# Kernel optimization log

Measured on AMD Instinct MI355X. Metric: run time of the kernel, lower is better.

## Reference

```python
import jax, jax.numpy as jnp
import numpy as np
import math

NUM_HEADS = 8
KEY_SIZE = 512
EMBED_DIM = 256
BN_EPS = 1e-5


def batchnorm2d_train(x, w, b):
    # x: [B, H, N, hd]; channel axis = 1 (heads). Training-mode batch stats
    # over (B, N, hd), biased variance, as in torch BatchNorm2d forward.
    mean = jnp.mean(x, axis=(0, 2, 3), keepdims=True)
    var = jnp.mean((x - mean) ** 2, axis=(0, 2, 3), keepdims=True)
    xn = (x - mean) * jax.lax.rsqrt(var + BN_EPS)
    return xn * w[None, :, None, None] + b[None, :, None, None]


def l2_normalize(x, axis, eps=1e-12):
    # matches F.normalize(p=2): x / max(||x||, eps)
    n = jnp.sqrt(jnp.sum(x * x, axis=axis, keepdims=True))
    return x / jnp.maximum(n, eps)


def sparsemax(z, axis):
    # Euclidean projection onto the simplex along `axis` (Martins & Astudillo).
    K = z.shape[axis]
    z = z - jnp.max(z, axis=axis, keepdims=True)  # shift-invariant, for stability
    zs = jnp.flip(jnp.sort(z, axis=axis), axis=axis)  # descending sort
    rng_shape = [1] * z.ndim
    rng_shape[axis] = K
    rng = jnp.arange(1, K + 1, dtype=z.dtype).reshape(rng_shape)
    css = jnp.cumsum(zs, axis=axis)
    support = (1.0 + rng * zs) > css
    k_z = jnp.sum(support.astype(jnp.int32), axis=axis, keepdims=True)  # support size >= 1
    tau_sum = jnp.take_along_axis(css, k_z - 1, axis=axis)
    tau = (tau_sum - 1.0) / k_z.astype(z.dtype)
    return jnp.maximum(z - tau, 0.0)


def setup_inputs() -> dict:
    key = jax.random.key(0)
    k1, k2, k3 = jax.random.split(key, 3)
    B, N, C = 8, 1024, EMBED_DIM
    lim = 1.0 / math.sqrt(C)  # torch Linear default init range
    x = jax.random.normal(k1, (B, N, C), dtype=jnp.float32)
    qw = jax.random.uniform(k2, (KEY_SIZE, C), jnp.float32, -lim, lim)
    kw = jax.random.uniform(k3, (KEY_SIZE, C), jnp.float32, -lim, lim)
    bn_weight = jnp.ones((NUM_HEADS,), jnp.float32)
    bn_bias = jnp.zeros((NUM_HEADS,), jnp.float32)
    return {"x": x, "qw": qw, "kw": kw, "bn_weight": bn_weight, "bn_bias": bn_bias}


def reference(x, qw, kw, bn_weight, bn_bias):
    B, N, C = x.shape
    H = NUM_HEADS
    hd = KEY_SIZE // H
    q = jnp.einsum('bnc,kc->bnk', x, qw)  # [B,N,key_size]
    k = jnp.einsum('bnc,kc->bnk', x, kw)
    Q = q.reshape(B, N, H, hd).transpose(0, 2, 1, 3)  # [B,H,N,hd]
    K = k.reshape(B, N, H, hd).transpose(0, 2, 1, 3)
    Q = batchnorm2d_train(Q, bn_weight, bn_bias)
    K = batchnorm2d_train(K, bn_weight, bn_bias)
    Q = l2_normalize(Q, axis=3)
    K = l2_normalize(K, axis=3)
    scores = jnp.einsum('bhnd,bhmd->bhnm', Q, K) / math.sqrt(C)  # scale by sqrt(embeded_dim)
    scores = scores.transpose(0, 2, 1, 3).reshape(B, N, H * N)  # [B,N,H*N]
    # dropout is identity in eval mode
    return sparsemax(scores, axis=1)
```

## Files before the change

### kernel.cpp

```cpp
#include <hip/hip_runtime.h>
#include <math.h>

#define S_STAT 0
#define S_Q    32
#define S_K    (32 + 4194304)
#define S_PL   (32 + 8388608)
#define PLSZ   4194304

typedef unsigned short ushort;
typedef unsigned int uint;
typedef __attribute__((ext_vector_type(8))) short short8;
typedef __attribute__((ext_vector_type(16))) float floatx16;

__device__ __forceinline__ float wave_sum(float v) {
#pragma unroll
    for (int m = 1; m < 64; m <<= 1) v += __shfl_xor(v, m);
    return v;
}

__device__ __forceinline__ ushort f2bf(float f) {
    uint u = __float_as_uint(f);
    uint r = (u + 0x7fffu + ((u >> 16) & 1u)) >> 16;
    return (ushort)r;
}

__global__ __launch_bounds__(64) void k0_zero(float* __restrict__ ws) {
    if (threadIdx.x < 32) ws[S_STAT + threadIdx.x] = 0.0f;
}

__global__ __launch_bounds__(256) void k1_gemm(const float* __restrict__ x,
                                               const float* __restrict__ qw,
                                               const float* __restrict__ kw,
                                               float* __restrict__ ws) {
    __shared__ float xa[64][20];
    __shared__ float wb[64][20];
    __shared__ float red[8];
    const int t  = threadIdx.x;
    const int n0 = blockIdx.x * 64;
    const int ty = blockIdx.y;
    const bool is_q = (ty < 8);
    const int j0 = (ty & 7) * 64;
    const float* __restrict__ W = is_q ? qw : kw;
    float* __restrict__ outp = ws + (is_q ? S_Q : S_K);

    const int lr = t >> 2;
    const int lc = (t & 3) * 4;
    const int tr = (t >> 4) * 4;
    const int tc = (t & 15) * 4;

    float acc[4][4];
#pragma unroll
    for (int i = 0; i < 4; ++i)
#pragma unroll
        for (int j = 0; j < 4; ++j) acc[i][j] = 0.0f;

    for (int kc = 0; kc < 256; kc += 16) {
        __syncthreads();
        *(float4*)(&xa[lr][lc]) = *(const float4*)(x + (size_t)(n0 + lr) * 256 + kc + lc);
        *(float4*)(&wb[lr][lc]) = *(const float4*)(W + (size_t)(j0 + lr) * 256 + kc + lc);
        __syncthreads();
#pragma unroll
        for (int k4 = 0; k4 < 16; k4 += 4) {
            float4 av[4], bv[4];
#pragma unroll
            for (int i = 0; i < 4; ++i) av[i] = *(const float4*)(&xa[tr + i][k4]);
#pragma unroll
            for (int j = 0; j < 4; ++j) bv[j] = *(const float4*)(&wb[tc + j][k4]);
#pragma unroll
            for (int i = 0; i < 4; ++i)
#pragma unroll
                for (int j = 0; j < 4; ++j)
                    acc[i][j] = fmaf(av[i].x, bv[j].x,
                                fmaf(av[i].y, bv[j].y,
                                fmaf(av[i].z, bv[j].z,
                                fmaf(av[i].w, bv[j].w, acc[i][j]))));
        }
    }
#pragma unroll
    for (int i = 0; i < 4; ++i) {
        float4 o = make_float4(acc[i][0], acc[i][1], acc[i][2], acc[i][3]);
        *(float4*)(outp + (size_t)(n0 + tr + i) * 512 + j0 + tc) = o;
    }
    float s1 = 0.0f, s2 = 0.0f;
#pragma unroll
    for (int i = 0; i < 4; ++i)
#pragma unroll
        for (int j = 0; j < 4; ++j) { s1 += acc[i][j]; s2 += acc[i][j] * acc[i][j]; }
    s1 = wave_sum(s1);
    s2 = wave_sum(s2);
    if ((t & 63) == 0) { red[t >> 6] = s1; red[4 + (t >> 6)] = s2; }
    __syncthreads();
    if (t == 0) {
        float t1 = red[0] + red[1] + red[2] + red[3];
        float t2 = red[4] + red[5] + red[6] + red[7];
        const int base = (is_q ? 0 : 16) + (ty & 7);
        atomicAdd(ws + S_STAT + base, t1);
        atomicAdd(ws + S_STAT + base + 8, t2);
    }
}

__global__ __launch_bounds__(256) void k3_norm(const float* __restrict__ bnw,
                                               const float* __restrict__ bnb,
                                               float* __restrict__ ws) {
    const int t = threadIdx.x;
    const int w = t >> 6, l = t & 63;
    const int nb = blockIdx.x;
    const int bh = blockIdx.y;
    const int b = bh >> 3, h = bh & 7;
    const int z = blockIdx.z;
    const float* __restrict__ in = ws + (z ? S_K : S_Q);
    const float* st = ws + S_STAT + (z ? 16 : 0);
    ushort* __restrict__ PH = (ushort*)(ws + S_PL) + (z ? 2 * PLSZ : 0) + (size_t)bh * 65536;
    ushort* __restrict__ PL = PH + PLSZ;
    const float inv_m = 1.0f / 524288.0f;
    const float mean  = st[h] * inv_m;
    const float var   = st[8 + h] * inv_m - mean * mean;
    const float alpha = rsqrtf(var + 1e-5f) * bnw[h];
    const float beta  = bnb[h] - mean * alpha;
    const float scale = z ? 0.0625f : 1.0f;

#pragma unroll 1
    for (int i = 0; i < 16; ++i) {
        const int n = nb * 64 + w * 16 + i;
        float v = in[(size_t)(b * 1024 + n) * 512 + h * 64 + l];
        v = fmaf(v, alpha, beta);
        float ss = wave_sum(v * v);
        v = v / fmaxf(sqrtf(ss), 1e-12f) * scale;
        ushort h16 = f2bf(v);
        float hif = __uint_as_float(((uint)h16) << 16);
        ushort l16 = f2bf(v - hif);
        const int idx = n * 64 + l;
        PH[idx] = h16;
        PL[idx] = l16;
    }
}

__global__ __launch_bounds__(256, 2) void k4_attn(const float* __restrict__ ws,
                                                  float* __restrict__ out) {
    __shared__ float part[4][4][32];
    const int t = threadIdx.x;
    const int l = t & 63;
    const int w = t >> 6;
    const int bid = blockIdx.x;
    const int bh = bid & 63;
    const int mt = bid >> 6;
    const int b = bh >> 3, h = bh & 7;
    const int m0 = mt * 32;
    const ushort* __restrict__ QH = (const ushort*)(ws + S_PL);
    const ushort* __restrict__ QL = QH + PLSZ;
    const ushort* __restrict__ KH = QH + 2 * PLSZ;
    const ushort* __restrict__ KL = QH + 3 * PLSZ;

    const int row = l & 31;
    const int kb8 = l >> 5;

    short8 kf[2][4];
#pragma unroll
    for (int ks = 0; ks < 4; ++ks) {
        const size_t off = (size_t)(bh * 1024 + m0 + row) * 64 + ks * 16 + kb8 * 8;
        kf[0][ks] = *(const short8*)(KH + off);
        kf[1][ks] = *(const short8*)(KL + off);
    }

    floatx16 acc[8] = {};

#pragma unroll
    for (int r = 0; r < 8; ++r) {
        const size_t qoff = (size_t)(bh * 1024 + w * 256 + r * 32 + row) * 64 + kb8 * 8;
#pragma unroll
        for (int ks = 0; ks < 4; ++ks) {
            short8 ah = *(const short8*)(QH + qoff + ks * 16);
            short8 al = *(const short8*)(QL + qoff + ks * 16);
            acc[r] = __builtin_amdgcn_mfma_f32_32x32x16_bf16(ah, kf[0][ks], acc[r], 0, 0, 0);
            acc[r] = __builtin_amdgcn_mfma_f32_32x32x16_bf16(al, kf[0][ks], acc[r], 0, 0, 0);
            acc[r] = __builtin_amdgcn_mfma_f32_32x32x16_bf16(ah, kf[1][ks], acc[r], 0, 0, 0);
        }
    }

    const int col = row;
    float vmaxl = -1e30f, vsuml = 0.f;
#pragma unroll
    for (int r = 0; r < 8; ++r)
#pragma unroll
        for (int e = 0; e < 16; ++e) {
            const float zz = acc[r][e];
            vmaxl = fmaxf(vmaxl, zz);
            vsuml += zz;
        }
    vmaxl = fmaxf(vmaxl, __shfl_xor(vmaxl, 32));
    vsuml += __shfl_xor(vsuml, 32);
    if (l < 32) { part[2][w][col] = vmaxl; part[3][w][col] = vsuml; }
    __syncthreads();
    float vmax = fmaxf(fmaxf(part[2][0][col], part[2][1][col]),
                       fmaxf(part[2][2][col], part[2][3][col]));
    float vsum = part[3][0][col] + part[3][1][col] + part[3][2][col] + part[3][3][col];

    float lo = fmaxf(vmax - 1.0f, (vsum - 1.0f) * (1.0f / 1024.0f));
    float hi = vmax - (1.0f / 1024.0f);
#pragma unroll 1
    for (int it = 0; it < 12; ++it) {
        const float mid = 0.5f * (lo + hi);
        float sl = 0.f;
#pragma unroll
        for (int r = 0; r < 8; ++r)
#pragma unroll
            for (int e = 0; e < 16; ++e) sl += fmaxf(acc[r][e] - mid, 0.f);
        sl += __shfl_xor(sl, 32);
        if (l < 32) part[it & 1][w][col] = sl;
        __syncthreads();
        const float s = part[it & 1][0][col] + part[it & 1][1][col]
                      + part[it & 1][2][col] + part[it & 1][3][col];
        if (s > 1.0f) lo = mid; else hi = mid;
    }
    float cntl = 0.f, ssml = 0.f;
#pragma unroll
    for (int r = 0; r < 8; ++r)
#pragma unroll
        for (int e = 0; e < 16; ++e) {
            const float zz = acc[r][e];
            if (zz > lo) { cntl += 1.f; ssml += zz; }
        }
    cntl += __shfl_xor(cntl, 32);
    ssml += __shfl_xor(ssml, 32);
    if (l < 32) { part[2][w][col] = cntl; part[3][w][col] = ssml; }
    __syncthreads();
    const float cnt  = part[2][0][col] + part[2][1][col] + part[2][2][col] + part[2][3][col];
    const float ssum = part[3][0][col] + part[3][1][col] + part[3][2][col] + part[3][3][col];
    const float tau = (ssum - 1.0f) / cnt;

    float* __restrict__ ob = out + (size_t)b * 1024 * 8192 + h * 1024 + m0 + col;
    const int nbase = w * 256 + 4 * kb8;
#pragma unroll
    for (int r = 0; r < 8; ++r)
#pragma unroll
        for (int e = 0; e < 16; ++e) {
            const int n = nbase + r * 32 + (e & 3) + 8 * (e >> 2);
            ob[(size_t)n * 8192] = fmaxf(acc[r][e] - tau, 0.f);
        }
}

extern "C" void kernel_launch(void* const* d_in, const int* in_sizes, int n_in,
                              void* d_out, int out_size, void* d_ws, size_t ws_size,
                              hipStream_t stream) {
    (void)in_sizes; (void)n_in; (void)out_size; (void)ws_size;
    const float* x   = (const float*)d_in[0];
    const float* qw  = (const float*)d_in[1];
    const float* kw  = (const float*)d_in[2];
    const float* bnw = (const float*)d_in[3];
    const float* bnb = (const float*)d_in[4];
    float* ws  = (float*)d_ws;
    float* out = (float*)d_out;

    hipLaunchKernelGGL(k0_zero, dim3(1), dim3(64), 0, stream, ws);
    hipLaunchKernelGGL(k1_gemm, dim3(128, 16), dim3(256), 0, stream, x, qw, kw, ws);
    hipLaunchKernelGGL(k3_norm, dim3(16, 64, 2), dim3(256), 0, stream, bnw, bnb, ws);
    hipLaunchKernelGGL(k4_attn, dim3(2048), dim3(256), 0, stream, ws, out);
}
```

Measured before the change: 493.1 us.

## Replace fp32 SIMT projection GEMM with split-bf16 MFMA GEMM

Adds a pre-pass that splits x and the Q/K weights into high and low bf16 parts. The projection GEMM now runs on MFMA 32x32x16 bf16 instructions using three products (hh, lh, hl) to keep close to fp32 accuracy. Operands are loaded straight from global memory without LDS staging, and the batchnorm statistics are gathered per wave. This aims to cut the cost of the fp32 FMA GEMM, at the price of an extra conversion kernel, extra workspace traffic and scattered output stores.

```diff
diff --git a/kernel.cpp b/kernel.cpp
--- a/kernel.cpp
+++ b/kernel.cpp
@@ -28,74 +28,100 @@
     if (threadIdx.x < 32) ws[S_STAT + threadIdx.x] = 0.0f;
 }
 
-__global__ __launch_bounds__(256) void k1_gemm(const float* __restrict__ x,
-                                               const float* __restrict__ qw,
-                                               const float* __restrict__ kw,
-                                               float* __restrict__ ws) {
-    __shared__ float xa[64][20];
-    __shared__ float wb[64][20];
-    __shared__ float red[8];
-    const int t  = threadIdx.x;
-    const int n0 = blockIdx.x * 64;
-    const int ty = blockIdx.y;
-    const bool is_q = (ty < 8);
-    const int j0 = (ty & 7) * 64;
-    const float* __restrict__ W = is_q ? qw : kw;
+__global__ __launch_bounds__(256) void k_pre(const float* __restrict__ x,
+                                             const float* __restrict__ qw,
+                                             const float* __restrict__ kw,
+                                             float* __restrict__ ws) {
+    ushort* base = (ushort*)(ws + S_PL) + 4 * PLSZ;
+    ushort* XH = base;
+    ushort* XL = XH + 2097152;
+    ushort* WH = XL + 2097152;
+    ushort* WL = WH + 262144;
+    const int bid = blockIdx.x;
+    const int tid = threadIdx.x;
+    const float* __restrict__ src;
+    ushort *dh, *dl;
+    int idx4;
+    if (bid < 2048)      { src = x;  dh = XH;           dl = XL;           idx4 = bid * 256 + tid; }
+    else if (bid < 2176) { src = qw; dh = WH;           dl = WL;           idx4 = (bid - 2048) * 256 + tid; }
+    else                 { src = kw; dh = WH + 131072;  dl = WL + 131072;  idx4 = (bid - 2176) * 256 + tid; }
+    const float4 v = *(const float4*)(src + (size_t)idx4 * 4);
+    ushort4 hv, lv;
+    {
+        hv.x = f2bf(v.x); lv.x = f2bf(v.x - __uint_as_float(((uint)hv.x) << 16));
+        hv.y = f2bf(v.y); lv.y = f2bf(v.y - __uint_as_float(((uint)hv.y) << 16));
+        hv.z = f2bf(v.z); lv.z = f2bf(v.z - __uint_as_float(((uint)hv.z) << 16));
+        hv.w = f2bf(v.w); lv.w = f2bf(v.w - __uint_as_float(((uint)hv.w) << 16));
+    }
+    *(ushort4*)(dh + (size_t)idx4 * 4) = hv;
+    *(ushort4*)(dl + (size_t)idx4 * 4) = lv;
+}
+
+__global__ __launch_bounds__(256, 2) void k1_mfma(float* __restrict__ ws) {
+    const ushort* base = (const ushort*)(ws + S_PL) + 4 * PLSZ;
+    const ushort* __restrict__ XH = base;
+    const ushort* __restrict__ XL = XH + 2097152;
+    const ushort* __restrict__ WH = XL + 2097152;
+    const ushort* __restrict__ WL = WH + 262144;
+    const int t = threadIdx.x;
+    const int l = t & 63;
+    const int w = t >> 6;
+    const int rw = w & 1, cw = w >> 1;
+    const int row0 = blockIdx.x * 128 + rw * 64;
+    const int col0 = blockIdx.y * 128 + cw * 64;
+    const int lane31 = l & 31;
+    const int kb8 = (l >> 5) * 8;
+
+    floatx16 acc[2][2] = {};
+#pragma unroll 4
+    for (int kc = 0; kc < 256; kc += 16) {
+        short8 ah[2], al[2], bh[2], bl[2];
+#pragma unroll
+        for (int rt = 0; rt < 2; ++rt) {
+            const size_t o = (size_t)(row0 + rt * 32 + lane31) * 256 + kc + kb8;
+            ah[rt] = *(const short8*)(XH + o);
+            al[rt] = *(const short8*)(XL + o);
+        }
+#pragma unroll
+        for (int ct = 0; ct < 2; ++ct) {
+            const size_t o = (size_t)(col0 + ct * 32 + lane31) * 256 + kc + kb8;
+            bh[ct] = *(const short8*)(WH + o);
+            bl[ct] = *(const short8*)(WL + o);
+        }
+#pragma unroll
+        for (int rt = 0; rt < 2; ++rt)
+#pragma unroll
+            for (int ct = 0; ct < 2; ++ct) {
+                acc[rt][ct] = __builtin_amdgcn_mfma_f32_32x32x16_bf16(ah[rt], bh[ct], acc[rt][ct], 0, 0, 0);
+                acc[rt][ct] = __builtin_amdgcn_mfma_f32_32x32x16_bf16(al[rt], bh[ct], acc[rt][ct], 0, 0, 0);
+                acc[rt][ct] = __builtin_amdgcn_mfma_f32_32x32x16_bf16(ah[rt], bl[ct], acc[rt][ct], 0, 0, 0);
+            }
+    }
+
+    const bool is_q = (col0 < 512);
     float* __restrict__ outp = ws + (is_q ? S_Q : S_K);
-
-    const int lr = t >> 2;
-    const int lc = (t & 3) * 4;
-    const int tr = (t >> 4) * 4;
-    const int tc = (t & 15) * 4;
-
-    float acc[4][4];
-#pragma unroll
-    for (int i = 0; i < 4; ++i)
-#pragma unroll
-        for (int j = 0; j < 4; ++j) acc[i][j] = 0.0f;
-
-    for (int kc = 0; kc < 256; kc += 16) {
-        __syncthreads();
-        *(float4*)(&xa[lr][lc]) = *(const float4*)(x + (size_t)(n0 + lr) * 256 + kc + lc);
-        *(float4*)(&wb[lr][lc]) = *(const float4*)(W + (size_t)(j0 + lr) * 256 + kc + lc);
-        __syncthreads();
-#pragma unroll
-        for (int k4 = 0; k4 < 16; k4 += 4) {
-            float4 av[4], bv[4];
-#pragma unroll
-            for (int i = 0; i < 4; ++i) av[i] = *(const float4*)(&xa[tr + i][k4]);
-#pragma unroll
-            for (int j = 0; j < 4; ++j) bv[j] = *(const float4*)(&wb[tc + j][k4]);
-#pragma unroll
-            for (int i = 0; i < 4; ++i)
-#pragma unroll
-                for (int j = 0; j < 4; ++j)
-                    acc[i][j] = fmaf(av[i].x, bv[j].x,
-                                fmaf(av[i].y, bv[j].y,
-                                fmaf(av[i].z, bv[j].z,
-                                fmaf(av[i].w, bv[j].w, acc[i][j]))));
-        }
-    }
-#pragma unroll
-    for (int i = 0; i < 4; ++i) {
-        float4 o = make_float4(acc[i][0], acc[i][1], acc[i][2], acc[i][3]);
-        *(float4*)(outp + (size_t)(n0 + tr + i) * 512 + j0 + tc) = o;
-    }
-    float s1 = 0.0f, s2 = 0.0f;
-#pragma unroll
-    for (int i = 0; i < 4; ++i)
-#pragma unroll
-        for (int j = 0; j < 4; ++j) { s1 += acc[i][j]; s2 += acc[i][j] * acc[i][j]; }
+    const int cbase = col0 & 511;
+    const int rsub = 4 * (l >> 5);
+    float s1 = 0.f, s2 = 0.f;
+#pragma unroll
+    for (int rt = 0; rt < 2; ++rt)
+#pragma unroll
+        for (int ct = 0; ct < 2; ++ct)
+#pragma unroll
+            for (int e = 0; e < 16; ++e) {
+                const int r = row0 + rt * 32 + rsub + (e & 3) + 8 * (e >> 2);
+                const int c = cbase + ct * 32 + lane31;
+                const float v = acc[rt][ct][e];
+                outp[(size_t)r * 512 + c] = v;
+                s1 += v; s2 += v * v;
+            }
     s1 = wave_sum(s1);
     s2 = wave_sum(s2);
-    if ((t & 63) == 0) { red[t >> 6] = s1; red[4 + (t >> 6)] = s2; }
-    __syncthreads();
-    if (t == 0) {
-        float t1 = red[0] + red[1] + red[2] + red[3];
-        float t2 = red[4] + red[5] + red[6] + red[7];
-        const int base = (is_q ? 0 : 16) + (ty & 7);
-        atomicAdd(ws + S_STAT + base, t1);
-        atomicAdd(ws + S_STAT + base + 8, t2);
+    if (l == 0) {
+        const int head = (cbase >> 6) & 7;
+        const int sb = (is_q ? 0 : 16) + head;
+        atomicAdd(ws + S_STAT + sb, s1);
+        atomicAdd(ws + S_STAT + sb + 8, s2);
     }
 }
 
@@ -252,7 +278,8 @@
     float* out = (float*)d_out;
 
     hipLaunchKernelGGL(k0_zero, dim3(1), dim3(64), 0, stream, ws);
-    hipLaunchKernelGGL(k1_gemm, dim3(128, 16), dim3(256), 0, stream, x, qw, kw, ws);
+    hipLaunchKernelGGL(k_pre, dim3(2304), dim3(256), 0, stream, x, qw, kw, ws);
+    hipLaunchKernelGGL(k1_mfma, dim3(64, 8), dim3(256), 0, stream, ws);
     hipLaunchKernelGGL(k3_norm, dim3(16, 64, 2), dim3(256), 0, stream, bnw, bnb, ws);
     hipLaunchKernelGGL(k4_attn, dim3(2048), dim3(256), 0, stream, ws, out);
 }
```

New measurement: 470.1 us. 4.7% less time.
